# Kernel tuning notes

Measured on AMD Instinct MI355X. Metric: run time of the kernel, lower is better.

## Reference

```python
import jax, jax.numpy as jnp
import numpy as np

D = 1024
H = 16
HD = D // H
EPS = 1e-5

def gelu_tanh(x):
    c = jnp.sqrt(jnp.asarray(2.0 / jnp.pi, x.dtype))
    return 0.5 * x * (1.0 + jnp.tanh(c * (x + 0.044715 * x ** 3)))

def layernorm(x, scale, shift):
    mean = x.mean(axis=-1, keepdims=True)
    var = x.var(axis=-1, keepdims=True)  # biased, matches unbiased=False
    return scale * (x - mean) / jnp.sqrt(var + EPS) + shift

def setup_inputs() -> dict:
    key = jax.random.key(0)
    ks = jax.random.split(key, 12)
    s = 0.02
    return {
        "x": jax.random.normal(ks[0], (2, 2048, D), jnp.float32),
        "Wq": jax.random.normal(ks[1], (D, D), jnp.float32) * s,
        "Wk": jax.random.normal(ks[2], (D, D), jnp.float32) * s,
        "Wv": jax.random.normal(ks[3], (D, D), jnp.float32) * s,
        "Wo": jax.random.normal(ks[4], (D, D), jnp.float32) * s,
        "bo": jnp.zeros((D,), jnp.float32),
        "W1": jax.random.normal(ks[5], (D, 4 * D), jnp.float32) * s,
        "b1": jnp.zeros((4 * D,), jnp.float32),
        "W2": jax.random.normal(ks[6], (4 * D, D), jnp.float32) * s,
        "b2": jnp.zeros((D,), jnp.float32),
        "g1": jnp.ones((D,), jnp.float32),
        "s1": jnp.zeros((D,), jnp.float32),
        "g2": jnp.ones((D,), jnp.float32),
        "s2": jnp.zeros((D,), jnp.float32),
    }

def reference(x, Wq, Wk, Wv, Wo, bo, W1, b1, W2, b2, g1, s1, g2, s2):
    B, S, _ = x.shape
    # --- attention sublayer (pre-LN) ---
    shortcut = x
    h = layernorm(x, g1, s1)
    q = (h @ Wq).reshape(B, S, H, HD).transpose(0, 2, 1, 3)  # bhsd
    k = (h @ Wk).reshape(B, S, H, HD).transpose(0, 2, 1, 3)
    v = (h @ Wv).reshape(B, S, H, HD).transpose(0, 2, 1, 3)
    scores = jnp.einsum('bhqd,bhkd->bhqk', q, k)
    causal = jnp.tril(jnp.ones((S, S), bool))
    scores = jnp.where(causal, scores, -jnp.inf)
    attn = jax.nn.softmax(scores / np.sqrt(HD), axis=-1)
    ctx = jnp.einsum('bhqk,bhkd->bhqd', attn, v)
    ctx = ctx.transpose(0, 2, 1, 3).reshape(B, S, D)
    x = ctx @ Wo + bo + shortcut
    # --- FFN sublayer (pre-LN) ---
    shortcut = x
    h = layernorm(x, g2, s2)
    h = gelu_tanh(h @ W1 + b1) @ W2 + b2
    return h + shortcut
```

## Files before the change

### kernel.cpp

```cpp
#include <hip/hip_runtime.h>
#include <hip/hip_bf16.h>
#include <math.h>

typedef __bf16 bf16;
typedef __bf16 bf16x4 __attribute__((ext_vector_type(4)));
typedef __bf16 bf16x8 __attribute__((ext_vector_type(8)));
typedef float f32x4 __attribute__((ext_vector_type(4)));

#define DEV static __device__ __forceinline__

constexpr int Dm = 1024;
constexpr int Sq = 2048;
constexpr int Mrows = 4096;
constexpr size_t AE = (size_t)Mrows * Dm;

DEV void gload_lds16(const void* g, void* l) {
  __builtin_amdgcn_global_load_lds((const __attribute__((address_space(1))) unsigned int*)g,
                                   (__attribute__((address_space(3))) unsigned int*)l,
                                   16, 0, 0);
}

DEV float gelu_f(float u) {
  const float c = 0.7978845608028654f;
  float t = c * (u + 0.044715f * u * u * u);
  return u / (1.0f + __expf(-2.0f * t));
}

__global__ void transpose_split_kernel(const float* __restrict__ W,
                                       bf16* __restrict__ Thi,
                                       int K, int N) {
  __shared__ float tile[64][65];
  const int t = threadIdx.x;
  const int nt = blockIdx.x * 64, kt = blockIdx.y * 64;
  #pragma unroll
  for (int i = 0; i < 16; ++i) {
    int id = i * 256 + t;
    int r = id >> 6, c = id & 63;
    tile[r][c] = W[(size_t)(kt + r) * N + nt + c];
  }
  __syncthreads();
  #pragma unroll
  for (int i = 0; i < 16; ++i) {
    int id = i * 256 + t;
    int n = id >> 6, k = id & 63;
    Thi[(size_t)(nt + n) * K + kt + k] = (bf16)tile[k][n];
  }
}

__global__ void ln_split_kernel(const float* __restrict__ x,
                                const float* __restrict__ gamma, const float* __restrict__ beta,
                                bf16* __restrict__ ohi, bf16* __restrict__ olo) {
  const int row = blockIdx.x, t = threadIdx.x;
  const float4 v = ((const float4*)(x + (size_t)row * Dm))[t];
  float s = v.x + v.y + v.z + v.w;
  float sq = v.x * v.x + v.y * v.y + v.z * v.z + v.w * v.w;
  #pragma unroll
  for (int off = 1; off < 64; off <<= 1) {
    s += __shfl_xor(s, off);
    sq += __shfl_xor(sq, off);
  }
  __shared__ float red[8];
  const int wave = t >> 6, lane = t & 63;
  if (lane == 0) { red[wave] = s; red[4 + wave] = sq; }
  __syncthreads();
  s = red[0] + red[1] + red[2] + red[3];
  sq = red[4] + red[5] + red[6] + red[7];
  const float mean = s * (1.0f / 1024.0f);
  const float var = sq * (1.0f / 1024.0f) - mean * mean;
  const float inv = 1.0f / sqrtf(var + 1e-5f);
  const float4 g4 = ((const float4*)gamma)[t];
  const float4 b4 = ((const float4*)beta)[t];
  float y[4];
  y[0] = (v.x - mean) * inv * g4.x + b4.x;
  y[1] = (v.y - mean) * inv * g4.y + b4.y;
  y[2] = (v.z - mean) * inv * g4.z + b4.z;
  y[3] = (v.w - mean) * inv * g4.w + b4.w;
  bf16x4 hv, lv;
  #pragma unroll
  for (int i = 0; i < 4; ++i) {
    bf16 hi = (bf16)y[i];
    hv[i] = hi;
    lv[i] = (bf16)(y[i] - (float)hi);
  }
  ((bf16x4*)(ohi + (size_t)row * Dm))[t] = hv;
  ((bf16x4*)(olo + (size_t)row * Dm))[t] = lv;
}

template<int EP>
__global__ __launch_bounds__(256, 4) void gemm_kernel(
    const bf16* __restrict__ Ahi, const bf16* __restrict__ Alo,
    const bf16* __restrict__ Bthi,
    int K, int N,
    bf16* __restrict__ Ohi, bf16* __restrict__ Olo,
    float* __restrict__ Of,
    const float* __restrict__ bias, const float* __restrict__ resid) {
  const int t = threadIdx.x, wave = t >> 6, lane = t & 63;
  const int wr = wave >> 1, wc = wave & 1;
  const int l15 = lane & 15, l4 = lane >> 4;
  const int nwg = gridDim.x * gridDim.y;
  const int p0 = blockIdx.y * gridDim.x + blockIdx.x;
  const int swz = (p0 & 7) * (nwg >> 3) + (p0 >> 3);
  const int row0 = (swz / gridDim.x) * 64, col0 = (swz % gridDim.x) * 128;

  __shared__ __align__(16) bf16 sAh[64 * 64], sAl[64 * 64];
  __shared__ __align__(16) bf16 sBh[128 * 64];

  f32x4 acc[2][4];
  #pragma unroll
  for (int m = 0; m < 2; ++m)
    #pragma unroll
    for (int n = 0; n < 4; ++n)
      acc[m][n] = (f32x4){0.f, 0.f, 0.f, 0.f};

  for (int kt = 0; kt < K; kt += 64) {
    #pragma unroll
    for (int p = 0; p < 2; ++p) {
      int id = p * 256 + t;
      int r = id >> 3, c = id & 7;
      int cs = (c ^ (r & 7)) << 3;
      size_t ga = (size_t)(row0 + r) * K + kt + cs;
      gload_lds16(Ahi + ga, (char*)sAh + (p * 256 + wave * 64) * 16);
      gload_lds16(Alo + ga, (char*)sAl + (p * 256 + wave * 64) * 16);
    }
    #pragma unroll
    for (int p = 0; p < 4; ++p) {
      int id = p * 256 + t;
      int r = id >> 3, c = id & 7;
      int cs = (c ^ (r & 7)) << 3;
      gload_lds16(Bthi + (size_t)(col0 + r) * K + kt + cs,
                  (char*)sBh + (p * 256 + wave * 64) * 16);
    }
    __syncthreads();

    bf16x8 afh[2][2], afl[2][2], bfh[4][2];
    #pragma unroll
    for (int m = 0; m < 2; ++m)
      #pragma unroll
      for (int ks = 0; ks < 2; ++ks) {
        int r = wr * 32 + m * 16 + l15;
        int ch = ((ks * 4 + l4) ^ (r & 7)) << 3;
        afh[m][ks] = *(const bf16x8*)&sAh[r * 64 + ch];
        afl[m][ks] = *(const bf16x8*)&sAl[r * 64 + ch];
      }
    #pragma unroll
    for (int n = 0; n < 4; ++n)
      #pragma unroll
      for (int ks = 0; ks < 2; ++ks) {
        int r = wc * 64 + n * 16 + l15;
        int ch = ((ks * 4 + l4) ^ (r & 7)) << 3;
        bfh[n][ks] = *(const bf16x8*)&sBh[r * 64 + ch];
      }
    #pragma unroll
    for (int ks = 0; ks < 2; ++ks)
      #pragma unroll
      for (int m = 0; m < 2; ++m)
        #pragma unroll
        for (int n = 0; n < 4; ++n)
          acc[m][n] = __builtin_amdgcn_mfma_f32_16x16x32_bf16(afh[m][ks], bfh[n][ks], acc[m][n], 0, 0, 0);
    #pragma unroll
    for (int ks = 0; ks < 2; ++ks)
      #pragma unroll
      for (int m = 0; m < 2; ++m)
        #pragma unroll
        for (int n = 0; n < 4; ++n)
          acc[m][n] = __builtin_amdgcn_mfma_f32_16x16x32_bf16(afl[m][ks], bfh[n][ks], acc[m][n], 0, 0, 0);
    __syncthreads();
  }

  #pragma unroll
  for (int m = 0; m < 2; ++m)
    #pragma unroll
    for (int n = 0; n < 4; ++n)
      #pragma unroll
      for (int rr = 0; rr < 4; ++rr) {
        int row = row0 + wr * 32 + m * 16 + l4 * 4 + rr;
        int col = col0 + wc * 64 + n * 16 + l15;
        float v = acc[m][n][rr];
        if constexpr (EP == 0) {
          int which = col >> 10;
          int c = col & 1023;
          if (which == 0) {
            float q = v * 0.18033688011111793f;
            bf16 hi = (bf16)q;
            size_t ad = (size_t)row * Dm + c;
            Ohi[ad] = hi; Ohi[AE + ad] = (bf16)(q - (float)hi);
          } else if (which == 1) {
            size_t ad = (size_t)row * Dm + c;
            Ohi[2 * AE + ad] = (bf16)v;
          } else {
            size_t ad = ((size_t)(row >> 11) * Dm + c) * Sq + (row & (Sq - 1));
            Ohi[4 * AE + ad] = (bf16)v;
          }
        } else if constexpr (EP == 1) {
          size_t ad = (size_t)row * N + col;
          Of[ad] = v + bias[col] + resid[ad];
        } else {
          float u = gelu_f(v + bias[col]);
          bf16 hi = (bf16)u;
          size_t ad = (size_t)row * N + col;
          Ohi[ad] = hi;
          Olo[ad] = (bf16)(u - (float)hi);
        }
      }
}

__global__ __launch_bounds__(256, 4) void attn_kernel(
    const bf16* __restrict__ qhi, const bf16* __restrict__ qlo,
    const bf16* __restrict__ khi, const bf16* __restrict__ vthi,
    bf16* __restrict__ chi, bf16* __restrict__ clo) {
  const int t = threadIdx.x, wave = t >> 6, lane = t & 63;
  const int l15 = lane & 15, l4 = lane >> 4;
  const int p0 = blockIdx.y * 16 + blockIdx.x;
  const int swz = (p0 & 7) * 64 + (p0 >> 3);
  const int bx = swz & 15, bh = swz >> 4;
  const int b = bh >> 4, h = bh & 15;

  __shared__ __align__(16) bf16 sK[2][4096], sV[2][4096], sP[4096];

  for (int half = 0; half < 2; ++half) {
    const int qt = (half == 0) ? (31 - bx) : bx;
    const int qb = qt * 64;
    const int q0 = qb + wave * 16;

    bf16x8 qfh[2], qfl[2];
    #pragma unroll
    for (int ks = 0; ks < 2; ++ks) {
      size_t ad = (size_t)(b * Sq + q0 + l15) * Dm + h * 64 + ks * 32 + l4 * 8;
      qfh[ks] = *(const bf16x8*)&qhi[ad];
      qfl[ks] = *(const bf16x8*)&qlo[ad];
    }

    f32x4 cacc[4];
    float mrun[4], lrun[4];
    #pragma unroll
    for (int nd = 0; nd < 4; ++nd) cacc[nd] = (f32x4){0.f, 0.f, 0.f, 0.f};
    #pragma unroll
    for (int rr = 0; rr < 4; ++rr) { mrun[rr] = -3e38f; lrun[rr] = 0.f; }

    auto STAGE = [&](int bb, int kb) {
      #pragma unroll
      for (int p = 0; p < 2; ++p) {
        int id = p * 256 + t;
        int r = id >> 3, c = id & 7;
        int cc = (c ^ (r & 7)) << 3;
        size_t ka = (size_t)(b * Sq + kb + r) * Dm + h * 64 + cc;
        size_t va = (size_t)(b * Dm + h * 64 + r) * Sq + kb + cc;
        gload_lds16(&khi[ka], (char*)&sK[bb][0] + (p * 256 + wave * 64) * 16);
        gload_lds16(&vthi[va], (char*)&sV[bb][0] + (p * 256 + wave * 64) * 16);
      }
    };

    STAGE(0, 0);
    __syncthreads();
    int cur = 0;

    for (int kb = 0; kb <= qb; kb += 64) {
      if (kb + 64 <= qb) STAGE(cur ^ 1, kb + 64);

      f32x4 sacc[4];
      #pragma unroll
      for (int nk = 0; nk < 4; ++nk) sacc[nk] = (f32x4){0.f, 0.f, 0.f, 0.f};
      {
        bf16x8 kf[4][2];
        #pragma unroll
        for (int nk = 0; nk < 4; ++nk)
          #pragma unroll
          for (int ks = 0; ks < 2; ++ks) {
            int r = nk * 16 + l15;
            int ch = ((ks * 4 + l4) ^ (r & 7)) << 3;
            kf[nk][ks] = *(const bf16x8*)&sK[cur][r * 64 + ch];
          }
        #pragma unroll
        for (int ks = 0; ks < 2; ++ks)
          #pragma unroll
          for (int nk = 0; nk < 4; ++nk)
            sacc[nk] = __builtin_amdgcn_mfma_f32_16x16x32_bf16(qfh[ks], kf[nk][ks], sacc[nk], 0, 0, 0);
        #pragma unroll
        for (int ks = 0; ks < 2; ++ks)
          #pragma unroll
          for (int nk = 0; nk < 4; ++nk)
            sacc[nk] = __builtin_amdgcn_mfma_f32_16x16x32_bf16(qfl[ks], kf[nk][ks], sacc[nk], 0, 0, 0);
      }

      const bool diag = (kb == qb);
      #pragma unroll
      for (int rr = 0; rr < 4; ++rr) {
        float mx = -3e38f;
        #pragma unroll
        for (int nk = 0; nk < 4; ++nk) {
          float tv = sacc[nk][rr];
          if (diag && (nk * 16 + l15 > wave * 16 + l4 * 4 + rr)) tv = -3e38f;
          sacc[nk][rr] = tv;
          mx = fmaxf(mx, tv);
        }
        mx = fmaxf(mx, __shfl_xor(mx, 1));
        mx = fmaxf(mx, __shfl_xor(mx, 2));
        mx = fmaxf(mx, __shfl_xor(mx, 4));
        mx = fmaxf(mx, __shfl_xor(mx, 8));
        float mold = mrun[rr];
        if (mx > mold + 8.0f) {
          float corr = exp2f(mold - mx);
          lrun[rr] *= corr;
          #pragma unroll
          for (int nd = 0; nd < 4; ++nd) cacc[nd][rr] *= corr;
          mrun[rr] = mx;
          mold = mx;
        }
        float rs = 0.f;
        #pragma unroll
        for (int nk = 0; nk < 4; ++nk) {
          float p = exp2f(sacc[nk][rr] - mold);
          sacc[nk][rr] = p;
          rs += p;
        }
        rs += __shfl_xor(rs, 1);
        rs += __shfl_xor(rs, 2);
        rs += __shfl_xor(rs, 4);
        rs += __shfl_xor(rs, 8);
        lrun[rr] += rs;
      }

      #pragma unroll
      for (int nk = 0; nk < 4; ++nk)
        #pragma unroll
        for (int rr = 0; rr < 4; ++rr) {
          int row = wave * 16 + l4 * 4 + rr;
          int col = nk * 16 + l15;
          int ad = row * 64 + (((col >> 3) ^ (row & 7)) << 3) + (col & 7);
          sP[ad] = (bf16)sacc[nk][rr];
        }

      {
        bf16x8 pf[2];
        #pragma unroll
        for (int ks = 0; ks < 2; ++ks) {
          int r = wave * 16 + l15;
          int ch = ((ks * 4 + l4) ^ (r & 7)) << 3;
          pf[ks] = *(const bf16x8*)&sP[r * 64 + ch];
        }
        bf16x8 vf[2][4];
        #pragma unroll
        for (int ks = 0; ks < 2; ++ks)
          #pragma unroll
          for (int nd = 0; nd < 4; ++nd) {
            int r = nd * 16 + l15;
            int ch = ((ks * 4 + l4) ^ (r & 7)) << 3;
            vf[ks][nd] = *(const bf16x8*)&sV[cur][r * 64 + ch];
          }
        #pragma unroll
        for (int ks = 0; ks < 2; ++ks)
          #pragma unroll
          for (int nd = 0; nd < 4; ++nd)
            cacc[nd] = __builtin_amdgcn_mfma_f32_16x16x32_bf16(pf[ks], vf[ks][nd], cacc[nd], 0, 0, 0);
      }
      __syncthreads();
      cur ^= 1;
    }

    #pragma unroll
    for (int rr = 0; rr < 4; ++rr) {
      float rcp = 1.0f / lrun[rr];
      int qr = q0 + l4 * 4 + rr;
      #pragma unroll
      for (int nd = 0; nd < 4; ++nd) {
        float ov = cacc[nd][rr] * rcp;
        size_t ad = (size_t)(b * Sq + qr) * Dm + h * 64 + nd * 16 + l15;
        bf16 hi = (bf16)ov;
        chi[ad] = hi;
        clo[ad] = (bf16)(ov - (float)hi);
      }
    }
  }
}

extern "C" void kernel_launch(void* const* d_in, const int* in_sizes, int n_in,
                              void* d_out, int out_size, void* d_ws, size_t ws_size,
                              hipStream_t stream) {
  const float* x  = (const float*)d_in[0];
  const float* Wq = (const float*)d_in[1];
  const float* Wk = (const float*)d_in[2];
  const float* Wv = (const float*)d_in[3];
  const float* Wo = (const float*)d_in[4];
  const float* bo = (const float*)d_in[5];
  const float* W1 = (const float*)d_in[6];
  const float* b1 = (const float*)d_in[7];
  const float* W2 = (const float*)d_in[8];
  const float* b2 = (const float*)d_in[9];
  const float* g1 = (const float*)d_in[10];
  const float* s1 = (const float*)d_in[11];
  const float* g2 = (const float*)d_in[12];
  const float* s2 = (const float*)d_in[13];
  float* out = (float*)d_out;

  if (ws_size < 150994944ULL) return;

  char* ws = (char*)d_ws;
  bf16* wqkvT_hi = (bf16*)(ws + 0);
  bf16* woT_hi   = (bf16*)(ws + 12582912);
  bf16* w1T_hi   = (bf16*)(ws + 16777216);
  bf16* w2T_hi   = (bf16*)(ws + 33554432);
  char* rA = ws + 50331648;
  bf16* h_hi  = (bf16*)(rA + 0);
  bf16* h_lo  = (bf16*)(rA + 8388608);
  bf16* q_hi  = (bf16*)(rA + 16777216);
  bf16* q_lo  = (bf16*)(rA + 25165824);
  bf16* k_hi  = (bf16*)(rA + 33554432);
  bf16* vT_hi = (bf16*)(rA + 50331648);
  bf16* a1_hi = (bf16*)(rA + 0);
  bf16* a1_lo = (bf16*)(rA + 33554432);
  char* rB = ws + 117440512;
  bf16* ctx_hi = (bf16*)(rB + 0);
  bf16* ctx_lo = (bf16*)(rB + 8388608);
  bf16* h2_hi  = (bf16*)(rB + 0);
  bf16* h2_lo  = (bf16*)(rB + 8388608);
  float* x1 = (float*)(ws + 134217728);

  transpose_split_kernel<<<dim3(16, 16), 256, 0, stream>>>(Wq, wqkvT_hi, 1024, 1024);
  transpose_split_kernel<<<dim3(16, 16), 256, 0, stream>>>(Wk, wqkvT_hi + 1024 * 1024, 1024, 1024);
  transpose_split_kernel<<<dim3(16, 16), 256, 0, stream>>>(Wv, wqkvT_hi + 2048 * 1024, 1024, 1024);
  transpose_split_kernel<<<dim3(16, 16), 256, 0, stream>>>(Wo, woT_hi, 1024, 1024);
  transpose_split_kernel<<<dim3(64, 16), 256, 0, stream>>>(W1, w1T_hi, 1024, 4096);
  transpose_split_kernel<<<dim3(16, 64), 256, 0, stream>>>(W2, w2T_hi, 4096, 1024);

  ln_split_kernel<<<4096, 256, 0, stream>>>(x, g1, s1, h_hi, h_lo);

  gemm_kernel<0><<<dim3(24, 64), 256, 0, stream>>>(h_hi, h_lo, wqkvT_hi,
                                                   1024, 3072, q_hi, nullptr, nullptr, nullptr, nullptr);
  attn_kernel<<<dim3(16, 32), 256, 0, stream>>>(q_hi, q_lo, k_hi, vT_hi, ctx_hi, ctx_lo);

  gemm_kernel<1><<<dim3(8, 64), 256, 0, stream>>>(ctx_hi, ctx_lo, woT_hi,
                                                  1024, 1024, nullptr, nullptr, x1, bo, x);
  ln_split_kernel<<<4096, 256, 0, stream>>>(x1, g2, s2, h2_hi, h2_lo);

  gemm_kernel<2><<<dim3(32, 64), 256, 0, stream>>>(h2_hi, h2_lo, w1T_hi,
                                                   1024, 4096, a1_hi, a1_lo, nullptr, b1, nullptr);
  gemm_kernel<1><<<dim3(8, 64), 256, 0, stream>>>(a1_hi, a1_lo, w2T_hi,
                                                  4096, 1024, nullptr, nullptr, out, b2, x1);
}
```

Measured before the change: 485.7 us.

## Drop bf16 hi/lo split for activations and remap attention grid per query tile

Removes the two-term bf16 (hi+lo) activation representation in the layernorm outputs, GEMM A-operands, GELU output and attention context, so each GEMM issues half the MFMAs and loads half the A tiles. The attention kernel now launches one block per (batch, head, query tile) instead of a block looping over two paired tiles, with an XCD-aware index mapping that interleaves long and short causal tiles. GEMM launch bounds rise to 6 waves per SIMD, which the smaller LDS footprint allows. Accuracy drops because activations are now single bf16, while Q keeps its hi/lo split.

```diff
diff --git a/kernel.cpp b/kernel.cpp
--- a/kernel.cpp
+++ b/kernel.cpp
@@ -47,9 +47,9 @@
   }
 }
 
-__global__ void ln_split_kernel(const float* __restrict__ x,
-                                const float* __restrict__ gamma, const float* __restrict__ beta,
-                                bf16* __restrict__ ohi, bf16* __restrict__ olo) {
+__global__ void ln_kernel(const float* __restrict__ x,
+                          const float* __restrict__ gamma, const float* __restrict__ beta,
+                          bf16* __restrict__ ohi) {
   const int row = blockIdx.x, t = threadIdx.x;
   const float4 v = ((const float4*)(x + (size_t)row * Dm))[t];
   float s = v.x + v.y + v.z + v.w;
@@ -70,28 +70,20 @@
   const float inv = 1.0f / sqrtf(var + 1e-5f);
   const float4 g4 = ((const float4*)gamma)[t];
   const float4 b4 = ((const float4*)beta)[t];
-  float y[4];
-  y[0] = (v.x - mean) * inv * g4.x + b4.x;
-  y[1] = (v.y - mean) * inv * g4.y + b4.y;
-  y[2] = (v.z - mean) * inv * g4.z + b4.z;
-  y[3] = (v.w - mean) * inv * g4.w + b4.w;
-  bf16x4 hv, lv;
-  #pragma unroll
-  for (int i = 0; i < 4; ++i) {
-    bf16 hi = (bf16)y[i];
-    hv[i] = hi;
-    lv[i] = (bf16)(y[i] - (float)hi);
-  }
+  bf16x4 hv;
+  hv[0] = (bf16)((v.x - mean) * inv * g4.x + b4.x);
+  hv[1] = (bf16)((v.y - mean) * inv * g4.y + b4.y);
+  hv[2] = (bf16)((v.z - mean) * inv * g4.z + b4.z);
+  hv[3] = (bf16)((v.w - mean) * inv * g4.w + b4.w);
   ((bf16x4*)(ohi + (size_t)row * Dm))[t] = hv;
-  ((bf16x4*)(olo + (size_t)row * Dm))[t] = lv;
 }
 
 template<int EP>
-__global__ __launch_bounds__(256, 4) void gemm_kernel(
-    const bf16* __restrict__ Ahi, const bf16* __restrict__ Alo,
+__global__ __launch_bounds__(256, 6) void gemm_kernel(
+    const bf16* __restrict__ Ahi,
     const bf16* __restrict__ Bthi,
     int K, int N,
-    bf16* __restrict__ Ohi, bf16* __restrict__ Olo,
+    bf16* __restrict__ Ohi,
     float* __restrict__ Of,
     const float* __restrict__ bias, const float* __restrict__ resid) {
   const int t = threadIdx.x, wave = t >> 6, lane = t & 63;
@@ -102,7 +94,7 @@
   const int swz = (p0 & 7) * (nwg >> 3) + (p0 >> 3);
   const int row0 = (swz / gridDim.x) * 64, col0 = (swz % gridDim.x) * 128;
 
-  __shared__ __align__(16) bf16 sAh[64 * 64], sAl[64 * 64];
+  __shared__ __align__(16) bf16 sAh[64 * 64];
   __shared__ __align__(16) bf16 sBh[128 * 64];
 
   f32x4 acc[2][4];
@@ -118,9 +110,8 @@
       int id = p * 256 + t;
       int r = id >> 3, c = id & 7;
       int cs = (c ^ (r & 7)) << 3;
-      size_t ga = (size_t)(row0 + r) * K + kt + cs;
-      gload_lds16(Ahi + ga, (char*)sAh + (p * 256 + wave * 64) * 16);
-      gload_lds16(Alo + ga, (char*)sAl + (p * 256 + wave * 64) * 16);
+      gload_lds16(Ahi + (size_t)(row0 + r) * K + kt + cs,
+                  (char*)sAh + (p * 256 + wave * 64) * 16);
     }
     #pragma unroll
     for (int p = 0; p < 4; ++p) {
@@ -132,7 +123,7 @@
     }
     __syncthreads();
 
-    bf16x8 afh[2][2], afl[2][2], bfh[4][2];
+    bf16x8 afh[2][2], bfh[4][2];
     #pragma unroll
     for (int m = 0; m < 2; ++m)
       #pragma unroll
@@ -140,7 +131,6 @@
         int r = wr * 32 + m * 16 + l15;
         int ch = ((ks * 4 + l4) ^ (r & 7)) << 3;
         afh[m][ks] = *(const bf16x8*)&sAh[r * 64 + ch];
-        afl[m][ks] = *(const bf16x8*)&sAl[r * 64 + ch];
       }
     #pragma unroll
     for (int n = 0; n < 4; ++n)
@@ -157,13 +147,6 @@
         #pragma unroll
         for (int n = 0; n < 4; ++n)
           acc[m][n] = __builtin_amdgcn_mfma_f32_16x16x32_bf16(afh[m][ks], bfh[n][ks], acc[m][n], 0, 0, 0);
-    #pragma unroll
-    for (int ks = 0; ks < 2; ++ks)
-      #pragma unroll
-      for (int m = 0; m < 2; ++m)
-        #pragma unroll
-        for (int n = 0; n < 4; ++n)
-          acc[m][n] = __builtin_amdgcn_mfma_f32_16x16x32_bf16(afl[m][ks], bfh[n][ks], acc[m][n], 0, 0, 0);
     __syncthreads();
   }
 
@@ -195,11 +178,8 @@
           size_t ad = (size_t)row * N + col;
           Of[ad] = v + bias[col] + resid[ad];
         } else {
-          float u = gelu_f(v + bias[col]);
-          bf16 hi = (bf16)u;
           size_t ad = (size_t)row * N + col;
-          Ohi[ad] = hi;
-          Olo[ad] = (bf16)(u - (float)hi);
+          Ohi[ad] = (bf16)gelu_f(v + bias[col]);
         }
       }
 }
@@ -207,168 +187,168 @@
 __global__ __launch_bounds__(256, 4) void attn_kernel(
     const bf16* __restrict__ qhi, const bf16* __restrict__ qlo,
     const bf16* __restrict__ khi, const bf16* __restrict__ vthi,
-    bf16* __restrict__ chi, bf16* __restrict__ clo) {
+    bf16* __restrict__ chi) {
   const int t = threadIdx.x, wave = t >> 6, lane = t & 63;
   const int l15 = lane & 15, l4 = lane >> 4;
-  const int p0 = blockIdx.y * 16 + blockIdx.x;
-  const int swz = (p0 & 7) * 64 + (p0 >> 3);
-  const int bx = swz & 15, bh = swz >> 4;
+  const int i = blockIdx.x;
+  const int xcd = i & 7, j = i >> 3;
+  const int hl = j & 3, qidx = j >> 2;
+  int qt;
+  if (qidx < 8)       qt = 31 - qidx;
+  else if (qidx < 16) qt = qidx - 8;
+  else if (qidx < 24) qt = 39 - qidx;
+  else                qt = qidx - 16;
+  const int bh = xcd * 4 + hl;
   const int b = bh >> 4, h = bh & 15;
+  const int qb = qt * 64;
+  const int q0 = qb + wave * 16;
 
   __shared__ __align__(16) bf16 sK[2][4096], sV[2][4096], sP[4096];
 
-  for (int half = 0; half < 2; ++half) {
-    const int qt = (half == 0) ? (31 - bx) : bx;
-    const int qb = qt * 64;
-    const int q0 = qb + wave * 16;
-
-    bf16x8 qfh[2], qfl[2];
-    #pragma unroll
-    for (int ks = 0; ks < 2; ++ks) {
-      size_t ad = (size_t)(b * Sq + q0 + l15) * Dm + h * 64 + ks * 32 + l4 * 8;
-      qfh[ks] = *(const bf16x8*)&qhi[ad];
-      qfl[ks] = *(const bf16x8*)&qlo[ad];
-    }
-
-    f32x4 cacc[4];
-    float mrun[4], lrun[4];
-    #pragma unroll
-    for (int nd = 0; nd < 4; ++nd) cacc[nd] = (f32x4){0.f, 0.f, 0.f, 0.f};
-    #pragma unroll
-    for (int rr = 0; rr < 4; ++rr) { mrun[rr] = -3e38f; lrun[rr] = 0.f; }
-
-    auto STAGE = [&](int bb, int kb) {
-      #pragma unroll
-      for (int p = 0; p < 2; ++p) {
-        int id = p * 256 + t;
-        int r = id >> 3, c = id & 7;
-        int cc = (c ^ (r & 7)) << 3;
-        size_t ka = (size_t)(b * Sq + kb + r) * Dm + h * 64 + cc;
-        size_t va = (size_t)(b * Dm + h * 64 + r) * Sq + kb + cc;
-        gload_lds16(&khi[ka], (char*)&sK[bb][0] + (p * 256 + wave * 64) * 16);
-        gload_lds16(&vthi[va], (char*)&sV[bb][0] + (p * 256 + wave * 64) * 16);
-      }
-    };
-
-    STAGE(0, 0);
+  bf16x8 qfh[2], qfl[2];
+  #pragma unroll
+  for (int ks = 0; ks < 2; ++ks) {
+    size_t ad = (size_t)(b * Sq + q0 + l15) * Dm + h * 64 + ks * 32 + l4 * 8;
+    qfh[ks] = *(const bf16x8*)&qhi[ad];
+    qfl[ks] = *(const bf16x8*)&qlo[ad];
+  }
+
+  f32x4 cacc[4];
+  float mrun[4], lrun[4];
+  #pragma unroll
+  for (int nd = 0; nd < 4; ++nd) cacc[nd] = (f32x4){0.f, 0.f, 0.f, 0.f};
+  #pragma unroll
+  for (int rr = 0; rr < 4; ++rr) { mrun[rr] = -3e38f; lrun[rr] = 0.f; }
+
+  auto STAGE = [&](int bb, int kb) {
+    #pragma unroll
+    for (int p = 0; p < 2; ++p) {
+      int id = p * 256 + t;
+      int r = id >> 3, c = id & 7;
+      int cc = (c ^ (r & 7)) << 3;
+      size_t ka = (size_t)(b * Sq + kb + r) * Dm + h * 64 + cc;
+      size_t va = (size_t)(b * Dm + h * 64 + r) * Sq + kb + cc;
+      gload_lds16(&khi[ka], (char*)&sK[bb][0] + (p * 256 + wave * 64) * 16);
+      gload_lds16(&vthi[va], (char*)&sV[bb][0] + (p * 256 + wave * 64) * 16);
+    }
+  };
+
+  STAGE(0, 0);
+  __syncthreads();
+  int cur = 0;
+
+  for (int kb = 0; kb <= qb; kb += 64) {
+    if (kb + 64 <= qb) STAGE(cur ^ 1, kb + 64);
+
+    f32x4 sacc[4];
+    #pragma unroll
+    for (int nk = 0; nk < 4; ++nk) sacc[nk] = (f32x4){0.f, 0.f, 0.f, 0.f};
+    {
+      bf16x8 kf[4][2];
+      #pragma unroll
+      for (int nk = 0; nk < 4; ++nk)
+        #pragma unroll
+        for (int ks = 0; ks < 2; ++ks) {
+          int r = nk * 16 + l15;
+          int ch = ((ks * 4 + l4) ^ (r & 7)) << 3;
+          kf[nk][ks] = *(const bf16x8*)&sK[cur][r * 64 + ch];
+        }
+      #pragma unroll
+      for (int ks = 0; ks < 2; ++ks)
+        #pragma unroll
+        for (int nk = 0; nk < 4; ++nk)
+          sacc[nk] = __builtin_amdgcn_mfma_f32_16x16x32_bf16(qfh[ks], kf[nk][ks], sacc[nk], 0, 0, 0);
+      #pragma unroll
+      for (int ks = 0; ks < 2; ++ks)
+        #pragma unroll
+        for (int nk = 0; nk < 4; ++nk)
+          sacc[nk] = __builtin_amdgcn_mfma_f32_16x16x32_bf16(qfl[ks], kf[nk][ks], sacc[nk], 0, 0, 0);
+    }
+
+    const bool diag = (kb == qb);
+    #pragma unroll
+    for (int rr = 0; rr < 4; ++rr) {
+      float mx = -3e38f;
+      #pragma unroll
+      for (int nk = 0; nk < 4; ++nk) {
+        float tv = sacc[nk][rr];
+        if (diag && (nk * 16 + l15 > wave * 16 + l4 * 4 + rr)) tv = -3e38f;
+        sacc[nk][rr] = tv;
+        mx = fmaxf(mx, tv);
+      }
+      mx = fmaxf(mx, __shfl_xor(mx, 1));
+      mx = fmaxf(mx, __shfl_xor(mx, 2));
+      mx = fmaxf(mx, __shfl_xor(mx, 4));
+      mx = fmaxf(mx, __shfl_xor(mx, 8));
+      float mold = mrun[rr];
+      if (mx > mold + 8.0f) {
+        float corr = exp2f(mold - mx);
+        lrun[rr] *= corr;
+        #pragma unroll
+        for (int nd = 0; nd < 4; ++nd) cacc[nd][rr] *= corr;
+        mrun[rr] = mx;
+        mold = mx;
+      }
+      float rs = 0.f;
+      #pragma unroll
+      for (int nk = 0; nk < 4; ++nk) {
+        float p = exp2f(sacc[nk][rr] - mold);
+        sacc[nk][rr] = p;
+        rs += p;
+      }
+      rs += __shfl_xor(rs, 1);
+      rs += __shfl_xor(rs, 2);
+      rs += __shfl_xor(rs, 4);
+      rs += __shfl_xor(rs, 8);
+      lrun[rr] += rs;
+    }
+
+    #pragma unroll
+    for (int nk = 0; nk < 4; ++nk)
+      #pragma unroll
+      for (int rr = 0; rr < 4; ++rr) {
+        int row = wave * 16 + l4 * 4 + rr;
+        int col = nk * 16 + l15;
+        int ad = row * 64 + (((col >> 3) ^ (row & 7)) << 3) + (col & 7);
+        sP[ad] = (bf16)sacc[nk][rr];
+      }
+
+    {
+      bf16x8 pf[2];
+      #pragma unroll
+      for (int ks = 0; ks < 2; ++ks) {
+        int r = wave * 16 + l15;
+        int ch = ((ks * 4 + l4) ^ (r & 7)) << 3;
+        pf[ks] = *(const bf16x8*)&sP[r * 64 + ch];
+      }
+      bf16x8 vf[2][4];
+      #pragma unroll
+      for (int ks = 0; ks < 2; ++ks)
+        #pragma unroll
+        for (int nd = 0; nd < 4; ++nd) {
+          int r = nd * 16 + l15;
+          int ch = ((ks * 4 + l4) ^ (r & 7)) << 3;
+          vf[ks][nd] = *(const bf16x8*)&sV[cur][r * 64 + ch];
+        }
+      #pragma unroll
+      for (int ks = 0; ks < 2; ++ks)
+        #pragma unroll
+        for (int nd = 0; nd < 4; ++nd)
+          cacc[nd] = __builtin_amdgcn_mfma_f32_16x16x32_bf16(pf[ks], vf[ks][nd], cacc[nd], 0, 0, 0);
+    }
     __syncthreads();
-    int cur = 0;
-
-    for (int kb = 0; kb <= qb; kb += 64) {
-      if (kb + 64 <= qb) STAGE(cur ^ 1, kb + 64);
-
-      f32x4 sacc[4];
-      #pragma unroll
-      for (int nk = 0; nk < 4; ++nk) sacc[nk] = (f32x4){0.f, 0.f, 0.f, 0.f};
-      {
-        bf16x8 kf[4][2];
-        #pragma unroll
-        for (int nk = 0; nk < 4; ++nk)
-          #pragma unroll
-          for (int ks = 0; ks < 2; ++ks) {
-            int r = nk * 16 + l15;
-            int ch = ((ks * 4 + l4) ^ (r & 7)) << 3;
-            kf[nk][ks] = *(const bf16x8*)&sK[cur][r * 64 + ch];
-          }
-        #pragma unroll
-        for (int ks = 0; ks < 2; ++ks)
-          #pragma unroll
-          for (int nk = 0; nk < 4; ++nk)
-            sacc[nk] = __builtin_amdgcn_mfma_f32_16x16x32_bf16(qfh[ks], kf[nk][ks], sacc[nk], 0, 0, 0);
-        #pragma unroll
-        for (int ks = 0; ks < 2; ++ks)
-          #pragma unroll
-          for (int nk = 0; nk < 4; ++nk)
-            sacc[nk] = __builtin_amdgcn_mfma_f32_16x16x32_bf16(qfl[ks], kf[nk][ks], sacc[nk], 0, 0, 0);
-      }
-
-      const bool diag = (kb == qb);
-      #pragma unroll
-      for (int rr = 0; rr < 4; ++rr) {
-        float mx = -3e38f;
-        #pragma unroll
-        for (int nk = 0; nk < 4; ++nk) {
-          float tv = sacc[nk][rr];
-          if (diag && (nk * 16 + l15 > wave * 16 + l4 * 4 + rr)) tv = -3e38f;
-          sacc[nk][rr] = tv;
-          mx = fmaxf(mx, tv);
-        }
-        mx = fmaxf(mx, __shfl_xor(mx, 1));
-        mx = fmaxf(mx, __shfl_xor(mx, 2));
-        mx = fmaxf(mx, __shfl_xor(mx, 4));
-        mx = fmaxf(mx, __shfl_xor(mx, 8));
-        float mold = mrun[rr];
-        if (mx > mold + 8.0f) {
-          float corr = exp2f(mold - mx);
-          lrun[rr] *= corr;
-          #pragma unroll
-          for (int nd = 0; nd < 4; ++nd) cacc[nd][rr] *= corr;
-          mrun[rr] = mx;
-          mold = mx;
-        }
-        float rs = 0.f;
-        #pragma unroll
-        for (int nk = 0; nk < 4; ++nk) {
-          float p = exp2f(sacc[nk][rr] - mold);
-          sacc[nk][rr] = p;
-          rs += p;
-        }
-        rs += __shfl_xor(rs, 1);
-        rs += __shfl_xor(rs, 2);
-        rs += __shfl_xor(rs, 4);
-        rs += __shfl_xor(rs, 8);
-        lrun[rr] += rs;
-      }
-
-      #pragma unroll
-      for (int nk = 0; nk < 4; ++nk)
-        #pragma unroll
-        for (int rr = 0; rr < 4; ++rr) {
-          int row = wave * 16 + l4 * 4 + rr;
-          int col = nk * 16 + l15;
-          int ad = row * 64 + (((col >> 3) ^ (row & 7)) << 3) + (col & 7);
-          sP[ad] = (bf16)sacc[nk][rr];
-        }
-
-      {
-        bf16x8 pf[2];
-        #pragma unroll
-        for (int ks = 0; ks < 2; ++ks) {
-          int r = wave * 16 + l15;
-          int ch = ((ks * 4 + l4) ^ (r & 7)) << 3;
-          pf[ks] = *(const bf16x8*)&sP[r * 64 + ch];
-        }
-        bf16x8 vf[2][4];
-        #pragma unroll
-        for (int ks = 0; ks < 2; ++ks)
-          #pragma unroll
-          for (int nd = 0; nd < 4; ++nd) {
-            int r = nd * 16 + l15;
-            int ch = ((ks * 4 + l4) ^ (r & 7)) << 3;
-            vf[ks][nd] = *(const bf16x8*)&sV[cur][r * 64 + ch];
-          }
-        #pragma unroll
-        for (int ks = 0; ks < 2; ++ks)
-          #pragma unroll
-          for (int nd = 0; nd < 4; ++nd)
-            cacc[nd] = __builtin_amdgcn_mfma_f32_16x16x32_bf16(pf[ks], vf[ks][nd], cacc[nd], 0, 0, 0);
-      }
-      __syncthreads();
-      cur ^= 1;
-    }
-
-    #pragma unroll
-    for (int rr = 0; rr < 4; ++rr) {
-      float rcp = 1.0f / lrun[rr];
-      int qr = q0 + l4 * 4 + rr;
-      #pragma unroll
-      for (int nd = 0; nd < 4; ++nd) {
-        float ov = cacc[nd][rr] * rcp;
-        size_t ad = (size_t)(b * Sq + qr) * Dm + h * 64 + nd * 16 + l15;
-        bf16 hi = (bf16)ov;
-        chi[ad] = hi;
-        clo[ad] = (bf16)(ov - (float)hi);
-      }
+    cur ^= 1;
+  }
+
+  #pragma unroll
+  for (int rr = 0; rr < 4; ++rr) {
+    float rcp = 1.0f / lrun[rr];
+    int qr = q0 + l4 * 4 + rr;
+    #pragma unroll
+    for (int nd = 0; nd < 4; ++nd) {
+      float ov = cacc[nd][rr] * rcp;
+      size_t ad = (size_t)(b * Sq + qr) * Dm + h * 64 + nd * 16 + l15;
+      chi[ad] = (bf16)ov;
     }
   }
 }
@@ -401,18 +381,14 @@
   bf16* w2T_hi   = (bf16*)(ws + 33554432);
   char* rA = ws + 50331648;
   bf16* h_hi  = (bf16*)(rA + 0);
-  bf16* h_lo  = (bf16*)(rA + 8388608);
   bf16* q_hi  = (bf16*)(rA + 16777216);
   bf16* q_lo  = (bf16*)(rA + 25165824);
   bf16* k_hi  = (bf16*)(rA + 33554432);
   bf16* vT_hi = (bf16*)(rA + 50331648);
   bf16* a1_hi = (bf16*)(rA + 0);
-  bf16* a1_lo = (bf16*)(rA + 33554432);
   char* rB = ws + 117440512;
   bf16* ctx_hi = (bf16*)(rB + 0);
-  bf16* ctx_lo = (bf16*)(rB + 8388608);
   bf16* h2_hi  = (bf16*)(rB + 0);
-  bf16* h2_lo  = (bf16*)(rB + 8388608);
   float* x1 = (float*)(ws + 134217728);
 
   transpose_split_kernel<<<dim3(16, 16), 256, 0, stream>>>(Wq, wqkvT_hi, 1024, 1024);
@@ -422,18 +398,18 @@
   transpose_split_kernel<<<dim3(64, 16), 256, 0, stream>>>(W1, w1T_hi, 1024, 4096);
   transpose_split_kernel<<<dim3(16, 64), 256, 0, stream>>>(W2, w2T_hi, 4096, 1024);
 
-  ln_split_kernel<<<4096, 256, 0, stream>>>(x, g1, s1, h_hi, h_lo);
-
-  gemm_kernel<0><<<dim3(24, 64), 256, 0, stream>>>(h_hi, h_lo, wqkvT_hi,
-                                                   1024, 3072, q_hi, nullptr, nullptr, nullptr, nullptr);
-  attn_kernel<<<dim3(16, 32), 256, 0, stream>>>(q_hi, q_lo, k_hi, vT_hi, ctx_hi, ctx_lo);
-
-  gemm_kernel<1><<<dim3(8, 64), 256, 0, stream>>>(ctx_hi, ctx_lo, woT_hi,
-                                                  1024, 1024, nullptr, nullptr, x1, bo, x);
-  ln_split_kernel<<<4096, 256, 0, stream>>>(x1, g2, s2, h2_hi, h2_lo);
-
-  gemm_kernel<2><<<dim3(32, 64), 256, 0, stream>>>(h2_hi, h2_lo, w1T_hi,
-                                                   1024, 4096, a1_hi, a1_lo, nullptr, b1, nullptr);
-  gemm_kernel<1><<<dim3(8, 64), 256, 0, stream>>>(a1_hi, a1_lo, w2T_hi,
-                                                  4096, 1024, nullptr, nullptr, out, b2, x1);
-}
+  ln_kernel<<<4096, 256, 0, stream>>>(x, g1, s1, h_hi);
+
+  gemm_kernel<0><<<dim3(24, 64), 256, 0, stream>>>(h_hi, wqkvT_hi,
+                                                   1024, 3072, q_hi, nullptr, nullptr, nullptr);
+  attn_kernel<<<dim3(1024), 256, 0, stream>>>(q_hi, q_lo, k_hi, vT_hi, ctx_hi);
+
+  gemm_kernel<1><<<dim3(8, 64), 256, 0, stream>>>(ctx_hi, woT_hi,
+                                                  1024, 1024, nullptr, x1, bo, x);
+  ln_kernel<<<4096, 256, 0, stream>>>(x1, g2, s2, h2_hi);
+
+  gemm_kernel<2><<<dim3(32, 64), 256, 0, stream>>>(h2_hi, w1T_hi,
+                                                   1024, 4096, a1_hi, nullptr, b1, nullptr);
+  gemm_kernel<1><<<dim3(8, 64), 256, 0, stream>>>(a1_hi, w2T_hi,
+                                                  4096, 1024, nullptr, out, b2, x1);
+}
```

Measured after the change: 408.4 us. -15.9%, faster.
